# Kernel tuning notes

Measured on AMD Instinct MI355X. Metric: run time of the kernel, lower is better.

## Reference

```python
import jax, jax.numpy as jnp
import numpy as np

N0, N1, N2 = 120000, 24000, 6000  # nodes per sampled layer
H1, C1 = 8, 64   # layer1: heads, nhid (concat -> 512)
H2, C2 = 8, 256  # layer2: out heads, code_embed_dim (mean over heads)
D = 256
NEG_SLOPE = 0.2


def gat_conv(x_src, x_dst, src, dst, W, att_src, att_dst, bias, n_tgt, concat):
    H, C = att_src.shape
    h_src = (x_src @ W).reshape(-1, H, C)   # [N_src, H, C]
    h_dst = (x_dst @ W).reshape(-1, H, C)   # [N_tgt, H, C]
    a_src = jnp.einsum('nhc,hc->nh', h_src, att_src)  # [N_src, H]
    a_dst = jnp.einsum('nhc,hc->nh', h_dst, att_dst)  # [N_tgt, H]
    e = a_src[src] + a_dst[dst]                       # [E, H]
    e = jnp.where(e > 0, e, NEG_SLOPE * e)            # LeakyReLU
    # segment softmax over edges grouped by target node
    m = jax.ops.segment_max(e, dst, num_segments=n_tgt)  # [N_tgt, H]
    ex = jnp.exp(e - m[dst])
    denom = jax.ops.segment_sum(ex, dst, num_segments=n_tgt)
    alpha = ex / denom[dst]                           # [E, H]
    msg = alpha[:, :, None] * h_src[src]              # [E, H, C]
    out = jax.ops.segment_sum(msg, dst, num_segments=n_tgt)  # [N_tgt, H, C]
    if concat:
        return out.reshape(n_tgt, H * C) + bias
    return out.mean(axis=1) + bias


def setup_inputs() -> dict:
    key = jax.random.key(0)
    ks = jax.random.split(key, 12)
    E1, E2 = 384000, 96000
    g1 = 1.0 / np.sqrt(D)
    g2 = 1.0 / np.sqrt(H1 * C1)
    return {
        'x': jax.random.normal(ks[0], (N0, D), jnp.float32),
        'src1': jax.random.randint(ks[1], (E1,), 0, N0),
        'dst1': jax.random.randint(ks[2], (E1,), 0, N1),
        'src2': jax.random.randint(ks[3], (E2,), 0, N1),
        'dst2': jax.random.randint(ks[4], (E2,), 0, N2),
        'W1': jax.random.normal(ks[5], (D, H1 * C1), jnp.float32) * g1,
        'att_src1': jax.random.normal(ks[6], (H1, C1), jnp.float32) * 0.1,
        'att_dst1': jax.random.normal(ks[7], (H1, C1), jnp.float32) * 0.1,
        'b1': jnp.zeros((H1 * C1,), jnp.float32),
        'W2': jax.random.normal(ks[8], (H1 * C1, H2 * C2), jnp.float32) * g2,
        'att_src2': jax.random.normal(ks[9], (H2, C2), jnp.float32) * 0.1,
        'att_dst2': jax.random.normal(ks[10], (H2, C2), jnp.float32) * 0.1,
        'b2': jnp.zeros((C2,), jnp.float32),
    }


def reference(x, src1, dst1, src2, dst2, W1, att_src1, att_dst1, b1,
              W2, att_src2, att_dst2, b2):
    # layer 1: bipartite conv (x, x[:N1]), concat heads, then ELU
    x1 = gat_conv(x, x[:N1], src1, dst1, W1, att_src1, att_dst1, b1, N1, True)
    x1 = jax.nn.elu(x1)
    # layer 2: (x1, x1[:N2]), mean over heads
    x2 = gat_conv(x1, x1[:N2], src2, dst2, W2, att_src2, att_dst2, b2, N2, False)
    return x2
```

## Files before the change

### kernel.cpp

```cpp
#include <hip/hip_runtime.h>
#include <hip/hip_bf16.h>
#include <cstdint>

typedef __attribute__((ext_vector_type(8))) short short8;
typedef __attribute__((ext_vector_type(4))) float floatx4;
typedef __hip_bfloat16 bf16;
typedef unsigned short u16;

static constexpr int cN0 = 120000, cN1 = 24000, cN2 = 6000;
static constexpr int cD = 256, cHC1 = 512;
static constexpr int CH1 = 4800;

__device__ __forceinline__ float dot4(float4 a, float4 b) {
  return a.x * b.x + a.y * b.y + a.z * b.z + a.w * b.w;
}

__global__ __launch_bounds__(256)
void gat_w1t(const float* __restrict__ W1, u16* __restrict__ dst) {
  int t = blockIdx.x * 256 + threadIdx.x;
  if (t >= 512 * 256) return;
  int n = t >> 8, k = t & 255;
  bf16 v = bf16(W1[(size_t)k * 512 + n]);
  dst[t] = *(u16*)&v;
}

__global__ __launch_bounds__(256)
void gat_make_w2te(const float* __restrict__ W2, u16* __restrict__ out) {
  __shared__ u16 tile[32][33];
  int kt = blockIdx.x * 32, ct = blockIdx.y * 32, h = blockIdx.z;
  int tx = threadIdx.x & 31, ty4 = (threadIdx.x >> 5) * 4;
#pragma unroll
  for (int i = 0; i < 4; i++) {
    int k = kt + ty4 + i, c = ct + tx;
    bf16 v = bf16(W2[(size_t)k * 2048 + h * 256 + c]);
    tile[ty4 + i][tx] = *(u16*)&v;
  }
  __syncthreads();
#pragma unroll
  for (int i = 0; i < 4; i++) {
    int c = ct + ty4 + i, k = kt + tx;
    out[(size_t)c * 4096 + h * 512 + k] = tile[tx][ty4 + i];
  }
}

__global__ __launch_bounds__(256)
void gat_make_watt(const float* __restrict__ W, const float* __restrict__ atts,
                   const float* __restrict__ attd, float* __restrict__ ws,
                   float* __restrict__ wd, int K, int Ch, int ldw) {
  int lane = threadIdx.x & 63;
  int task = blockIdx.x * 4 + (threadIdx.x >> 6);
  if (task >= 8 * K) return;
  int h = task / K, k = task - h * K;
  const float* Wr = W + (size_t)k * ldw + h * Ch;
  const float* as = atts + h * Ch;
  const float* ad = attd + h * Ch;
  float ss = 0.f, dd = 0.f;
  for (int c = lane; c < Ch; c += 64) {
    float wv = Wr[c];
    ss += wv * as[c];
    dd += wv * ad[c];
  }
#pragma unroll
  for (int o = 32; o; o >>= 1) { ss += __shfl_down(ss, o); dd += __shfl_down(dd, o); }
  if (lane == 0) { ws[task] = ss; wd[task] = dd; }
}

#define RSTAGE(HALF, MASK)                                              \
  {                                                                     \
    _Pragma("unroll") for (int j = 0; j < HALF; j++) {                  \
      float send = (lane & MASK) ? v[j] : v[j + HALF];                  \
      float rcv = __shfl_xor(send, MASK);                               \
      v[j] = ((lane & MASK) ? v[j + HALF] : v[j]) + rcv;                \
    }                                                                   \
  }

__global__ __launch_bounds__(256)
void gat_scores_reg(const float* __restrict__ x, const float* __restrict__ wsrc,
                    const float* __restrict__ wdst, float* __restrict__ a_s,
                    float* __restrict__ a_d, int M, int MD) {
  int lane = threadIdx.x & 63;
  int wv = (blockIdx.x * 256 + threadIdx.x) >> 6;
  int nw = (gridDim.x * 256) >> 6;
  float4 w[16];
#pragma unroll
  for (int j = 0; j < 8; j++) {
    w[j]     = *(const float4*)&wsrc[j * 256 + lane * 4];
    w[j + 8] = *(const float4*)&wdst[j * 256 + lane * 4];
  }
  for (int row = wv; row < M; row += nw) {
    float4 xv = *(const float4*)&x[(size_t)row * 256 + lane * 4];
    float v[16];
#pragma unroll
    for (int j = 0; j < 16; j++) v[j] = dot4(xv, w[j]);
    RSTAGE(8, 1) RSTAGE(4, 2) RSTAGE(2, 4) RSTAGE(1, 8)
    v[0] += __shfl_xor(v[0], 16);
    v[0] += __shfl_xor(v[0], 32);
    if (lane < 16) {
      int o = ((lane & 1) << 3) | ((lane & 2) << 1) | ((lane & 4) >> 1) | ((lane & 8) >> 3);
      if (o < 8) a_s[row * 8 + o] = v[0];
      else if (row < MD) a_d[row * 8 + (o - 8)] = v[0];
    }
  }
}

__global__ __launch_bounds__(256)
void gat_scores_w512(const float* __restrict__ x, const float* __restrict__ wsrc,
                     const float* __restrict__ wdst, float* __restrict__ a_s,
                     float* __restrict__ a_d, int M, int MD) {
  __shared__ float wl[16 * 512];
  int tid = threadIdx.x;
#pragma unroll
  for (int base = 0; base < 8192; base += 1024) {
    int idx = base + tid * 4;
    int j = idx >> 9, c = idx & 511;
    *(float4*)&wl[idx] = (j < 8) ? *(const float4*)&wsrc[j * 512 + c]
                                 : *(const float4*)&wdst[(j - 8) * 512 + c];
  }
  __syncthreads();
  int lane = tid & 63;
  int wv = (blockIdx.x * 256 + tid) >> 6;
  int nw = (gridDim.x * 256) >> 6;
  for (int row = wv; row < M; row += nw) {
    float4 xa = *(const float4*)&x[(size_t)row * 512 + lane * 4];
    float4 xb = *(const float4*)&x[(size_t)row * 512 + 256 + lane * 4];
    float v[16];
#pragma unroll
    for (int j = 0; j < 16; j++) {
      float4 wa = *(const float4*)&wl[j * 512 + lane * 4];
      float4 wb = *(const float4*)&wl[j * 512 + 256 + lane * 4];
      v[j] = dot4(xa, wa) + dot4(xb, wb);
    }
    RSTAGE(8, 1) RSTAGE(4, 2) RSTAGE(2, 4) RSTAGE(1, 8)
    v[0] += __shfl_xor(v[0], 16);
    v[0] += __shfl_xor(v[0], 32);
    if (lane < 16) {
      int o = ((lane & 1) << 3) | ((lane & 2) << 1) | ((lane & 4) >> 1) | ((lane & 8) >> 3);
      if (o < 8) a_s[row * 8 + o] = v[0];
      else if (row < MD) a_d[row * 8 + (o - 8)] = v[0];
    }
  }
}

__global__ __launch_bounds__(256)
void gat_hist(const int* __restrict__ dstv, int* __restrict__ cnt, int E) {
  int t = blockIdx.x * 256 + threadIdx.x;
  if (t < E) atomicAdd(&cnt[dstv[t]], 1);
}

__global__ __launch_bounds__(1024)
void gat_scan_excl(const int* __restrict__ cnt, int* __restrict__ off, int n) {
  __shared__ int wsum[16];
  __shared__ int carry_s;
  int t = threadIdx.x, lane = t & 63, wid = t >> 6;
  if (t == 0) carry_s = 0;
  __syncthreads();
  for (int base = 0; base < n; base += 1024) {
    int idx = base + t;
    int v = (idx < n) ? cnt[idx] : 0;
    int x = v;
#pragma unroll
    for (int d = 1; d < 64; d <<= 1) { int y = __shfl_up(x, d); if (lane >= d) x += y; }
    if (lane == 63) wsum[wid] = x;
    __syncthreads();
    if (t < 16) {
      int s = wsum[t];
#pragma unroll
      for (int d = 1; d < 16; d <<= 1) { int y = __shfl_up(s, d); if (t >= d) s += y; }
      wsum[t] = s;
    }
    __syncthreads();
    int prefix = carry_s + (wid ? wsum[wid - 1] : 0) + x - v;
    if (idx < n) off[idx] = prefix;
    int tot = wsum[15];
    __syncthreads();
    if (t == 0) carry_s += tot;
    __syncthreads();
  }
  if (threadIdx.x == 0) off[n] = carry_s;
}

__global__ __launch_bounds__(256)
void gat_scatter_edge(const int* __restrict__ src, const int* __restrict__ dstv,
                      const float* __restrict__ a_s, const float* __restrict__ a_d,
                      const int* __restrict__ off, int* __restrict__ cur,
                      int* __restrict__ srcs, float* __restrict__ exs, int E) {
  int t = blockIdx.x * 256 + threadIdx.x;
  if (t >= E) return;
  int s = src[t], d = dstv[t];
  int slot = off[d] + atomicAdd(&cur[d], 1);
  srcs[slot] = s;
  const float* as = a_s + (size_t)s * 8;
  const float* ad = a_d + (size_t)d * 8;
  float4 s0 = *(const float4*)as, s1 = *(const float4*)(as + 4);
  float4 d0 = *(const float4*)ad, d1 = *(const float4*)(ad + 4);
  float ev[8] = { s0.x + d0.x, s0.y + d0.y, s0.z + d0.z, s0.w + d0.w,
                  s1.x + d1.x, s1.y + d1.y, s1.z + d1.z, s1.w + d1.w };
  float exv[8];
#pragma unroll
  for (int h = 0; h < 8; h++) {
    float e = ev[h];
    e = e > 0.f ? e : 0.2f * e;
    exv[h] = expf(e);
  }
  float4* op = (float4*)(exs + (size_t)slot * 8);
  op[0] = make_float4(exv[0], exv[1], exv[2], exv[3]);
  op[1] = make_float4(exv[4], exv[5], exv[6], exv[7]);
}

__global__ __launch_bounds__(256)
void gat_denom(const float* __restrict__ exs, const int* __restrict__ off,
               float* __restrict__ den, int N) {
  int lane = threadIdx.x & 63;
  int d = blockIdx.x * 4 + (threadIdx.x >> 6);
  if (d >= N) return;
  int beg = off[d], end = off[d + 1];
  float s = 0.f;
  for (size_t idx = (size_t)beg * 8 + lane; idx < (size_t)end * 8; idx += 64)
    s += exs[idx];
#pragma unroll
  for (int o = 32; o >= 8; o >>= 1) s += __shfl_down(s, o);
  if (lane < 8) den[(size_t)d * 8 + lane] = s;
}

__global__ __launch_bounds__(256)
void gat_gather_in1(const float* __restrict__ x, const float* __restrict__ exs,
                    const float* __restrict__ den, const int* __restrict__ off,
                    const int* __restrict__ srcs, u16* __restrict__ agg, int d0) {
  int d = d0 + blockIdx.x, t = threadIdx.x;
  int beg = off[d], end = off[d + 1];
  float inv[8];
#pragma unroll
  for (int j = 0; j < 8; j++) inv[j] = 1.f / den[(size_t)d * 8 + j];
  float acc[8] = {};
  int s_n = 0;
  if (beg < end) s_n = srcs[beg];
  for (int i = beg; i < end; i++) {
    int s = s_n;
    if (i + 1 < end) s_n = srcs[i + 1];
    float4 e0 = *(const float4*)&exs[(size_t)i * 8];
    float4 e1 = *(const float4*)&exs[(size_t)i * 8 + 4];
    float xv = x[(size_t)s * cD + t];
    acc[0] += e0.x * inv[0] * xv; acc[1] += e0.y * inv[1] * xv;
    acc[2] += e0.z * inv[2] * xv; acc[3] += e0.w * inv[3] * xv;
    acc[4] += e1.x * inv[4] * xv; acc[5] += e1.y * inv[5] * xv;
    acc[6] += e1.z * inv[6] * xv; acc[7] += e1.w * inv[7] * xv;
  }
  u16* ap = agg + (size_t)blockIdx.x * 2048 + t;
#pragma unroll
  for (int j = 0; j < 8; j++) {
    bf16 v = bf16(acc[j]);
    ap[(size_t)j * 256] = *(u16*)&v;
  }
}

__global__ __launch_bounds__(256)
void gat_gather_in2(const float* __restrict__ x1, const float* __restrict__ exs,
                    const float* __restrict__ den, const int* __restrict__ off,
                    const int* __restrict__ srcs, u16* __restrict__ agg, int d0) {
  int d = d0 + blockIdx.x, t = threadIdx.x;
  int beg = off[d], end = off[d + 1];
  float inv[8];
#pragma unroll
  for (int j = 0; j < 8; j++) inv[j] = 1.f / den[(size_t)d * 8 + j];
  float acc0[8] = {}, acc1[8] = {};
  int s_n = 0;
  if (beg < end) s_n = srcs[beg];
  for (int i = beg; i < end; i++) {
    int s = s_n;
    if (i + 1 < end) s_n = srcs[i + 1];
    float4 e0 = *(const float4*)&exs[(size_t)i * 8];
    float4 e1 = *(const float4*)&exs[(size_t)i * 8 + 4];
    float al[8] = { e0.x * inv[0], e0.y * inv[1], e0.z * inv[2], e0.w * inv[3],
                    e1.x * inv[4], e1.y * inv[5], e1.z * inv[6], e1.w * inv[7] };
    float xv0 = x1[(size_t)s * cHC1 + t];
    float xv1 = x1[(size_t)s * cHC1 + t + 256];
#pragma unroll
    for (int j = 0; j < 8; j++) { acc0[j] += al[j] * xv0; acc1[j] += al[j] * xv1; }
  }
  u16* ap = agg + (size_t)blockIdx.x * 4096;
#pragma unroll
  for (int j = 0; j < 8; j++) {
    bf16 v0 = bf16(acc0[j]), v1 = bf16(acc1[j]);
    ap[(size_t)j * 512 + t]       = *(u16*)&v0;
    ap[(size_t)j * 512 + t + 256] = *(u16*)&v1;
  }
}

template<int BN, int EPI>
__global__ __launch_bounds__(256)
void gat_gemm(const u16* __restrict__ A, long lda, const u16* __restrict__ Bt, long ldb,
              float* __restrict__ C, long ldc, int M, int K,
              const float* __restrict__ bias, int zA, int zB, long zC, int zBias) {
  __shared__ __align__(16) u16 Al[64 * 64];
  __shared__ __align__(16) u16 Bl[BN * 64];
  const int tid = threadIdx.x;
  const int bm = blockIdx.x << 6;
  const int n0 = blockIdx.y * BN;
  const int z = blockIdx.z;
  const u16* Ab = A + (size_t)z * zA;
  const u16* Bb = Bt + (size_t)z * zB + (size_t)n0 * ldb;
  const int wid = tid >> 6, lane = tid & 63;
  const int wm = (wid & 1) << 5, wn = (wid >> 1) * (BN / 2);
  const int q = lane >> 4, r = lane & 15;
  constexpr int NJ = BN / 32;
  floatx4 acc[2][NJ] = {};
  const int arow = tid >> 3;
  const int chunk = tid & 7;
  const int acol = chunk << 3;
  for (int k0 = 0; k0 < K; k0 += 64) {
    __syncthreads();
#pragma unroll
    for (int rr = 0; rr < 2; rr++) {
      int row = arow + rr * 32;
      int gr = bm + row; if (gr >= M) gr = M - 1;
      *(uint4*)&Al[row * 64 + ((chunk ^ (row & 7)) << 3)] =
          *(const uint4*)&Ab[(size_t)gr * lda + k0 + acol];
    }
#pragma unroll
    for (int rr = 0; rr < BN / 32; rr++) {
      int row = arow + rr * 32;
      *(uint4*)&Bl[row * 64 + ((chunk ^ (row & 7)) << 3)] =
          *(const uint4*)&Bb[(size_t)row * ldb + k0 + acol];
    }
    __syncthreads();
#pragma unroll
    for (int kk = 0; kk < 64; kk += 32) {
      const int cs = (((kk >> 3) + q) ^ (r & 7)) << 3;
      short8 af[2], bfr[NJ];
#pragma unroll
      for (int i = 0; i < 2; i++)  af[i]  = *(const short8*)&Al[(wm + i * 16 + r) * 64 + cs];
#pragma unroll
      for (int j = 0; j < NJ; j++) bfr[j] = *(const short8*)&Bl[(wn + j * 16 + r) * 64 + cs];
#pragma unroll
      for (int i = 0; i < 2; i++)
#pragma unroll
        for (int j = 0; j < NJ; j++)
          acc[i][j] = __builtin_amdgcn_mfma_f32_16x16x32_bf16(af[i], bfr[j], acc[i][j], 0, 0, 0);
    }
  }
#pragma unroll
  for (int i = 0; i < 2; i++)
#pragma unroll
    for (int j = 0; j < NJ; j++) {
      int gn = n0 + wn + j * 16 + r;
      float bv = (EPI == 1) ? bias[zBias * z + gn] : 0.f;
#pragma unroll
      for (int t2 = 0; t2 < 4; t2++) {
        int gm = bm + wm + i * 16 + q * 4 + t2;
        if (gm < M) {
          float v = acc[i][j][t2];
          if (EPI == 1) { v += bv; v = v > 0.f ? v : expm1f(v); }
          C[(size_t)z * zC + (size_t)gm * ldc + gn] = v;
        }
      }
    }
}

__global__ __launch_bounds__(256)
void gat_reduce4(const float* __restrict__ p, const float* __restrict__ bias,
                 float* __restrict__ out, int MN) {
  int t = blockIdx.x * 256 + threadIdx.x;
  if (t >= MN) return;
  size_t mn = (size_t)MN;
  float v = p[t] + p[t + mn] + p[t + 2 * mn] + p[t + 3 * mn];
  out[t] = v * 0.125f + bias[t & 255];
}

extern "C" void kernel_launch(void* const* d_in, const int* in_sizes, int n_in,
                              void* d_out, int out_size, void* d_ws, size_t ws_size,
                              hipStream_t stream) {
  const float* x    = (const float*)d_in[0];
  const int* src1   = (const int*)d_in[1];
  const int* dst1   = (const int*)d_in[2];
  const int* src2   = (const int*)d_in[3];
  const int* dst2   = (const int*)d_in[4];
  const float* W1   = (const float*)d_in[5];
  const float* atts1 = (const float*)d_in[6];
  const float* attd1 = (const float*)d_in[7];
  const float* b1   = (const float*)d_in[8];
  const float* W2   = (const float*)d_in[9];
  const float* atts2 = (const float*)d_in[10];
  const float* attd2 = (const float*)d_in[11];
  const float* b2   = (const float*)d_in[12];
  const int E1 = in_sizes[1], E2 = in_sizes[3];

  uint8_t* p = (uint8_t*)d_ws;
  auto alloc = [&](size_t b) { uint8_t* r = p; p += (b + 255) & ~(size_t)255; return r; };
  auto al = [](size_t b) { return (b + 255) & ~(size_t)255; };
  float* x1   = (float*)alloc((size_t)cN1 * cHC1 * 4);
  u16*   W1t  = (u16*)alloc((size_t)512 * 256 * 2);
  u16*   W2te = (u16*)alloc((size_t)256 * 4096 * 2);
  float* wts1 = (float*)alloc(8 * 256 * 4);
  float* wtd1 = (float*)alloc(8 * 256 * 4);
  float* wts2 = (float*)alloc(8 * 512 * 4);
  float* wtd2 = (float*)alloc(8 * 512 * 4);
  uint8_t* scratch = p;
  u16*   aggA  = (u16*)alloc((size_t)CH1 * 2048 * 2);
  float* a_s1  = (float*)alloc((size_t)cN0 * 32);
  float* a_d1  = (float*)alloc((size_t)cN1 * 32);
  float* exs1  = (float*)alloc((size_t)E1 * 32);
  int*   srcs1 = (int*)alloc((size_t)E1 * 4);
  int*   off1  = (int*)alloc((size_t)(cN1 + 1) * 4);
  float* den1  = (float*)alloc((size_t)cN1 * 32);
  uint8_t* zA = p;
  int*   cnt1 = (int*)alloc((size_t)cN1 * 4);
  int*   cur1 = (int*)alloc((size_t)cN1 * 4);
  size_t zAbytes = (size_t)(p - zA);

  size_t fixedB = al((size_t)cN1 * 32) + al((size_t)cN2 * 32) + al((size_t)E2 * 32) +
                  al((size_t)E2 * 4) + al((size_t)(cN2 + 1) * 4) + al((size_t)cN2 * 32) +
                  2 * al((size_t)cN2 * 4);
  size_t usedPersist = (size_t)(scratch - (uint8_t*)d_ws);
  int M2 = 6000;
  if (usedPersist + al((size_t)6000 * 4096 * 2) + al(4ull * 6000 * 256 * 4) + fixedB > ws_size)
    M2 = 3000;
  int nch2 = 6000 / M2;
  p = scratch;
  u16*   aggB  = (u16*)alloc((size_t)M2 * 4096 * 2);
  float* pbuf  = (float*)alloc(4ull * M2 * 256 * 4);
  float* a_s2  = (float*)alloc((size_t)cN1 * 32);
  float* a_d2  = (float*)alloc((size_t)cN2 * 32);
  float* exs2  = (float*)alloc((size_t)E2 * 32);
  int*   srcs2 = (int*)alloc((size_t)E2 * 4);
  int*   off2  = (int*)alloc((size_t)(cN2 + 1) * 4);
  float* den2  = (float*)alloc((size_t)cN2 * 32);
  uint8_t* zB = p;
  int*   cnt2 = (int*)alloc((size_t)cN2 * 4);
  int*   cur2 = (int*)alloc((size_t)cN2 * 4);
  size_t zBbytes = (size_t)(p - zB);

  gat_w1t<<<(512 * 256 + 255) / 256, 256, 0, stream>>>(W1, W1t);
  gat_make_w2te<<<dim3(16, 8, 8), 256, 0, stream>>>(W2, W2te);
  gat_make_watt<<<2 * 256, 256, 0, stream>>>(W1, atts1, attd1, wts1, wtd1, 256, 64, 512);
  gat_make_watt<<<2 * 512, 256, 0, stream>>>(W2, atts2, attd2, wts2, wtd2, 512, 256, 2048);

  hipMemsetAsync(zA, 0, zAbytes, stream);
  gat_scores_reg<<<1024, 256, 0, stream>>>(x, wts1, wtd1, a_s1, a_d1, cN0, cN1);
  gat_hist<<<(E1 + 255) / 256, 256, 0, stream>>>(dst1, cnt1, E1);
  gat_scan_excl<<<1, 1024, 0, stream>>>(cnt1, off1, cN1);
  gat_scatter_edge<<<(E1 + 255) / 256, 256, 0, stream>>>(src1, dst1, a_s1, a_d1, off1, cur1, srcs1, exs1, E1);
  gat_denom<<<(cN1 + 3) / 4, 256, 0, stream>>>(exs1, off1, den1, cN1);
  for (int c = 0; c < cN1 / CH1; c++) {
    int d0 = c * CH1;
    gat_gather_in1<<<CH1, 256, 0, stream>>>(x, exs1, den1, off1, srcs1, aggA, d0);
    gat_gemm<64, 1><<<dim3(CH1 / 64, 1, 8), 256, 0, stream>>>(
        aggA, 2048, W1t, 256, x1 + (size_t)d0 * cHC1, cHC1,
        CH1, 256, b1, 256, 64 * 256, 64, 64);
  }

  hipMemsetAsync(zB, 0, zBbytes, stream);
  gat_scores_w512<<<512, 256, 0, stream>>>(x1, wts2, wtd2, a_s2, a_d2, cN1, cN2);
  gat_hist<<<(E2 + 255) / 256, 256, 0, stream>>>(dst2, cnt2, E2);
  gat_scan_excl<<<1, 1024, 0, stream>>>(cnt2, off2, cN2);
  gat_scatter_edge<<<(E2 + 255) / 256, 256, 0, stream>>>(src2, dst2, a_s2, a_d2, off2, cur2, srcs2, exs2, E2);
  gat_denom<<<(cN2 + 3) / 4, 256, 0, stream>>>(exs2, off2, den2, cN2);
  for (int c = 0; c < nch2; c++) {
    int d0 = c * M2;
    gat_gather_in2<<<M2, 256, 0, stream>>>(x1, exs2, den2, off2, srcs2, aggB, d0);
    gat_gemm<64, 0><<<dim3((M2 + 63) / 64, 4, 4), 256, 0, stream>>>(
        aggB, 4096, W2te, 4096, pbuf, 256,
        M2, 1024, nullptr, 1024, 1024, (long)M2 * 256, 0);
    gat_reduce4<<<(M2 * 256 + 255) / 256, 256, 0, stream>>>(
        pbuf, b2, (float*)d_out + (size_t)d0 * 256, M2 * 256);
  }
}
```

Measured before the change: 600.5 us.

## Parallelize scan, fuse softmax denominator into gather, unroll edges, enlarge chunks

Replaces the single-block serial prefix scan with a three-kernel multi-block scan. Drops the separate denominator kernel and accumulates the softmax denominator inside the gather loops, which now process two edges per iteration for more memory-level parallelism. Layer 1 runs as a single chunk when the workspace allows it, cutting launch count, and the layer-2 GEMM uses a 128-wide N tile. The cost is more registers in the gather kernels, plus a dependence on the workspace size check for the larger buffers.

```diff
diff --git a/kernel.cpp b/kernel.cpp
--- a/kernel.cpp
+++ b/kernel.cpp
@@ -148,35 +148,44 @@
 }
 
 __global__ __launch_bounds__(1024)
-void gat_scan_excl(const int* __restrict__ cnt, int* __restrict__ off, int n) {
+void gat_scan1(const int* __restrict__ cnt, int* __restrict__ off,
+               int* __restrict__ bsum, int n) {
   __shared__ int wsum[16];
-  __shared__ int carry_s;
   int t = threadIdx.x, lane = t & 63, wid = t >> 6;
-  if (t == 0) carry_s = 0;
+  int idx = blockIdx.x * 1024 + t;
+  int v = (idx < n) ? cnt[idx] : 0;
+  int x = v;
+#pragma unroll
+  for (int d = 1; d < 64; d <<= 1) { int y = __shfl_up(x, d); if (lane >= d) x += y; }
+  if (lane == 63) wsum[wid] = x;
   __syncthreads();
-  for (int base = 0; base < n; base += 1024) {
-    int idx = base + t;
-    int v = (idx < n) ? cnt[idx] : 0;
-    int x = v;
-#pragma unroll
-    for (int d = 1; d < 64; d <<= 1) { int y = __shfl_up(x, d); if (lane >= d) x += y; }
-    if (lane == 63) wsum[wid] = x;
-    __syncthreads();
-    if (t < 16) {
-      int s = wsum[t];
-#pragma unroll
-      for (int d = 1; d < 16; d <<= 1) { int y = __shfl_up(s, d); if (t >= d) s += y; }
-      wsum[t] = s;
-    }
-    __syncthreads();
-    int prefix = carry_s + (wid ? wsum[wid - 1] : 0) + x - v;
-    if (idx < n) off[idx] = prefix;
-    int tot = wsum[15];
-    __syncthreads();
-    if (t == 0) carry_s += tot;
-    __syncthreads();
-  }
-  if (threadIdx.x == 0) off[n] = carry_s;
+  if (t < 16) {
+    int s = wsum[t];
+#pragma unroll
+    for (int d = 1; d < 16; d <<= 1) { int y = __shfl_up(s, d); if (t >= d) s += y; }
+    wsum[t] = s;
+  }
+  __syncthreads();
+  int excl = (wid ? wsum[wid - 1] : 0) + x - v;
+  if (idx < n) off[idx] = excl;
+  if (t == 1023) bsum[blockIdx.x] = wsum[15];
+}
+
+__global__ __launch_bounds__(64)
+void gat_scan2(int* __restrict__ bsum, int nb, int* __restrict__ off, int n) {
+  int t = threadIdx.x;
+  int v = (t < nb) ? bsum[t] : 0;
+  int x = v;
+#pragma unroll
+  for (int d = 1; d < 64; d <<= 1) { int y = __shfl_up(x, d); if (t >= d) x += y; }
+  if (t < nb) bsum[t] = x - v;
+  if (t == 63) off[n] = x;
+}
+
+__global__ __launch_bounds__(256)
+void gat_scan3(int* __restrict__ off, const int* __restrict__ bsum, int n) {
+  int i = blockIdx.x * 256 + threadIdx.x;
+  if (i < n) off[i] += bsum[i >> 10];
 }
 
 __global__ __launch_bounds__(256)
@@ -208,79 +217,89 @@
 }
 
 __global__ __launch_bounds__(256)
-void gat_denom(const float* __restrict__ exs, const int* __restrict__ off,
-               float* __restrict__ den, int N) {
-  int lane = threadIdx.x & 63;
-  int d = blockIdx.x * 4 + (threadIdx.x >> 6);
-  if (d >= N) return;
-  int beg = off[d], end = off[d + 1];
-  float s = 0.f;
-  for (size_t idx = (size_t)beg * 8 + lane; idx < (size_t)end * 8; idx += 64)
-    s += exs[idx];
-#pragma unroll
-  for (int o = 32; o >= 8; o >>= 1) s += __shfl_down(s, o);
-  if (lane < 8) den[(size_t)d * 8 + lane] = s;
-}
-
-__global__ __launch_bounds__(256)
 void gat_gather_in1(const float* __restrict__ x, const float* __restrict__ exs,
-                    const float* __restrict__ den, const int* __restrict__ off,
-                    const int* __restrict__ srcs, u16* __restrict__ agg, int d0) {
+                    const int* __restrict__ off, const int* __restrict__ srcs,
+                    u16* __restrict__ agg, int d0) {
   int d = d0 + blockIdx.x, t = threadIdx.x;
   int beg = off[d], end = off[d + 1];
-  float inv[8];
-#pragma unroll
-  for (int j = 0; j < 8; j++) inv[j] = 1.f / den[(size_t)d * 8 + j];
-  float acc[8] = {};
-  int s_n = 0;
-  if (beg < end) s_n = srcs[beg];
-  for (int i = beg; i < end; i++) {
-    int s = s_n;
-    if (i + 1 < end) s_n = srcs[i + 1];
-    float4 e0 = *(const float4*)&exs[(size_t)i * 8];
-    float4 e1 = *(const float4*)&exs[(size_t)i * 8 + 4];
+  float acc[8] = {}, den[8] = {};
+  int i = beg;
+  if ((end - beg) & 1) {
+    int s = srcs[i];
+    float ea[8];
+    *(float4*)&ea[0] = *(const float4*)&exs[(size_t)i * 8];
+    *(float4*)&ea[4] = *(const float4*)&exs[(size_t)i * 8 + 4];
     float xv = x[(size_t)s * cD + t];
-    acc[0] += e0.x * inv[0] * xv; acc[1] += e0.y * inv[1] * xv;
-    acc[2] += e0.z * inv[2] * xv; acc[3] += e0.w * inv[3] * xv;
-    acc[4] += e1.x * inv[4] * xv; acc[5] += e1.y * inv[5] * xv;
-    acc[6] += e1.z * inv[6] * xv; acc[7] += e1.w * inv[7] * xv;
+#pragma unroll
+    for (int j = 0; j < 8; j++) { acc[j] += ea[j] * xv; den[j] += ea[j]; }
+    i++;
+  }
+  for (; i < end; i += 2) {
+    int s0 = srcs[i], s1 = srcs[i + 1];
+    float ea[8], eb[8];
+    *(float4*)&ea[0] = *(const float4*)&exs[(size_t)i * 8];
+    *(float4*)&ea[4] = *(const float4*)&exs[(size_t)i * 8 + 4];
+    *(float4*)&eb[0] = *(const float4*)&exs[(size_t)(i + 1) * 8];
+    *(float4*)&eb[4] = *(const float4*)&exs[(size_t)(i + 1) * 8 + 4];
+    float xv0 = x[(size_t)s0 * cD + t];
+    float xv1 = x[(size_t)s1 * cD + t];
+#pragma unroll
+    for (int j = 0; j < 8; j++) {
+      acc[j] += ea[j] * xv0 + eb[j] * xv1;
+      den[j] += ea[j] + eb[j];
+    }
   }
   u16* ap = agg + (size_t)blockIdx.x * 2048 + t;
 #pragma unroll
   for (int j = 0; j < 8; j++) {
-    bf16 v = bf16(acc[j]);
+    float inv = den[j] > 0.f ? 1.f / den[j] : 0.f;
+    bf16 v = bf16(acc[j] * inv);
     ap[(size_t)j * 256] = *(u16*)&v;
   }
 }
 
 __global__ __launch_bounds__(256)
 void gat_gather_in2(const float* __restrict__ x1, const float* __restrict__ exs,
-                    const float* __restrict__ den, const int* __restrict__ off,
-                    const int* __restrict__ srcs, u16* __restrict__ agg, int d0) {
+                    const int* __restrict__ off, const int* __restrict__ srcs,
+                    u16* __restrict__ agg, int d0) {
   int d = d0 + blockIdx.x, t = threadIdx.x;
   int beg = off[d], end = off[d + 1];
-  float inv[8];
-#pragma unroll
-  for (int j = 0; j < 8; j++) inv[j] = 1.f / den[(size_t)d * 8 + j];
-  float acc0[8] = {}, acc1[8] = {};
-  int s_n = 0;
-  if (beg < end) s_n = srcs[beg];
-  for (int i = beg; i < end; i++) {
-    int s = s_n;
-    if (i + 1 < end) s_n = srcs[i + 1];
-    float4 e0 = *(const float4*)&exs[(size_t)i * 8];
-    float4 e1 = *(const float4*)&exs[(size_t)i * 8 + 4];
-    float al[8] = { e0.x * inv[0], e0.y * inv[1], e0.z * inv[2], e0.w * inv[3],
-                    e1.x * inv[4], e1.y * inv[5], e1.z * inv[6], e1.w * inv[7] };
-    float xv0 = x1[(size_t)s * cHC1 + t];
-    float xv1 = x1[(size_t)s * cHC1 + t + 256];
-#pragma unroll
-    for (int j = 0; j < 8; j++) { acc0[j] += al[j] * xv0; acc1[j] += al[j] * xv1; }
+  float acc0[8] = {}, acc1[8] = {}, den[8] = {};
+  int i = beg;
+  if ((end - beg) & 1) {
+    int s = srcs[i];
+    float ea[8];
+    *(float4*)&ea[0] = *(const float4*)&exs[(size_t)i * 8];
+    *(float4*)&ea[4] = *(const float4*)&exs[(size_t)i * 8 + 4];
+    float xa = x1[(size_t)s * cHC1 + t];
+    float xb = x1[(size_t)s * cHC1 + t + 256];
+#pragma unroll
+    for (int j = 0; j < 8; j++) { acc0[j] += ea[j] * xa; acc1[j] += ea[j] * xb; den[j] += ea[j]; }
+    i++;
+  }
+  for (; i < end; i += 2) {
+    int s0 = srcs[i], s1 = srcs[i + 1];
+    float ea[8], eb[8];
+    *(float4*)&ea[0] = *(const float4*)&exs[(size_t)i * 8];
+    *(float4*)&ea[4] = *(const float4*)&exs[(size_t)i * 8 + 4];
+    *(float4*)&eb[0] = *(const float4*)&exs[(size_t)(i + 1) * 8];
+    *(float4*)&eb[4] = *(const float4*)&exs[(size_t)(i + 1) * 8 + 4];
+    float xa0 = x1[(size_t)s0 * cHC1 + t];
+    float xb0 = x1[(size_t)s0 * cHC1 + t + 256];
+    float xa1 = x1[(size_t)s1 * cHC1 + t];
+    float xb1 = x1[(size_t)s1 * cHC1 + t + 256];
+#pragma unroll
+    for (int j = 0; j < 8; j++) {
+      acc0[j] += ea[j] * xa0 + eb[j] * xa1;
+      acc1[j] += ea[j] * xb0 + eb[j] * xb1;
+      den[j] += ea[j] + eb[j];
+    }
   }
   u16* ap = agg + (size_t)blockIdx.x * 4096;
 #pragma unroll
   for (int j = 0; j < 8; j++) {
-    bf16 v0 = bf16(acc0[j]), v1 = bf16(acc1[j]);
+    float inv = den[j] > 0.f ? 1.f / den[j] : 0.f;
+    bf16 v0 = bf16(acc0[j] * inv), v1 = bf16(acc1[j] * inv);
     ap[(size_t)j * 512 + t]       = *(u16*)&v0;
     ap[(size_t)j * 512 + t + 256] = *(u16*)&v1;
   }
@@ -395,25 +414,33 @@
   float* wts2 = (float*)alloc(8 * 512 * 4);
   float* wtd2 = (float*)alloc(8 * 512 * 4);
   uint8_t* scratch = p;
-  u16*   aggA  = (u16*)alloc((size_t)CH1 * 2048 * 2);
+  size_t usedPersist = (size_t)(scratch - (uint8_t*)d_ws);
+
+  auto phaseA = [&](size_t m1) {
+    return al(m1 * 2048 * 2) + al((size_t)cN0 * 32) + al((size_t)cN1 * 32) +
+           al((size_t)E1 * 32) + al((size_t)E1 * 4) + al((size_t)(cN1 + 1) * 4) +
+           al(256) + 2 * al((size_t)cN1 * 4);
+  };
+  int M1 = (usedPersist + phaseA(cN1) <= ws_size) ? cN1 : CH1;
+  int nch1 = cN1 / M1;
+  u16*   aggA  = (u16*)alloc((size_t)M1 * 2048 * 2);
   float* a_s1  = (float*)alloc((size_t)cN0 * 32);
   float* a_d1  = (float*)alloc((size_t)cN1 * 32);
   float* exs1  = (float*)alloc((size_t)E1 * 32);
   int*   srcs1 = (int*)alloc((size_t)E1 * 4);
   int*   off1  = (int*)alloc((size_t)(cN1 + 1) * 4);
-  float* den1  = (float*)alloc((size_t)cN1 * 32);
+  int*   bsum1 = (int*)alloc(256);
   uint8_t* zA = p;
   int*   cnt1 = (int*)alloc((size_t)cN1 * 4);
   int*   cur1 = (int*)alloc((size_t)cN1 * 4);
   size_t zAbytes = (size_t)(p - zA);
 
-  size_t fixedB = al((size_t)cN1 * 32) + al((size_t)cN2 * 32) + al((size_t)E2 * 32) +
-                  al((size_t)E2 * 4) + al((size_t)(cN2 + 1) * 4) + al((size_t)cN2 * 32) +
-                  2 * al((size_t)cN2 * 4);
-  size_t usedPersist = (size_t)(scratch - (uint8_t*)d_ws);
-  int M2 = 6000;
-  if (usedPersist + al((size_t)6000 * 4096 * 2) + al(4ull * 6000 * 256 * 4) + fixedB > ws_size)
-    M2 = 3000;
+  auto phaseB = [&](size_t m2) {
+    return al(m2 * 4096 * 2) + al(4ull * m2 * 256 * 4) + al((size_t)cN1 * 32) +
+           al((size_t)cN2 * 32) + al((size_t)E2 * 32) + al((size_t)E2 * 4) +
+           al((size_t)(cN2 + 1) * 4) + al(256) + 2 * al((size_t)cN2 * 4);
+  };
+  int M2 = (usedPersist + phaseB(6000) <= ws_size) ? 6000 : 3000;
   int nch2 = 6000 / M2;
   p = scratch;
   u16*   aggB  = (u16*)alloc((size_t)M2 * 4096 * 2);
@@ -423,7 +450,7 @@
   float* exs2  = (float*)alloc((size_t)E2 * 32);
   int*   srcs2 = (int*)alloc((size_t)E2 * 4);
   int*   off2  = (int*)alloc((size_t)(cN2 + 1) * 4);
-  float* den2  = (float*)alloc((size_t)cN2 * 32);
+  int*   bsum2 = (int*)alloc(256);
   uint8_t* zB = p;
   int*   cnt2 = (int*)alloc((size_t)cN2 * 4);
   int*   cur2 = (int*)alloc((size_t)cN2 * 4);
@@ -437,27 +464,35 @@
   hipMemsetAsync(zA, 0, zAbytes, stream);
   gat_scores_reg<<<1024, 256, 0, stream>>>(x, wts1, wtd1, a_s1, a_d1, cN0, cN1);
   gat_hist<<<(E1 + 255) / 256, 256, 0, stream>>>(dst1, cnt1, E1);
-  gat_scan_excl<<<1, 1024, 0, stream>>>(cnt1, off1, cN1);
+  {
+    int nb = (cN1 + 1023) / 1024;
+    gat_scan1<<<nb, 1024, 0, stream>>>(cnt1, off1, bsum1, cN1);
+    gat_scan2<<<1, 64, 0, stream>>>(bsum1, nb, off1, cN1);
+    gat_scan3<<<(cN1 + 255) / 256, 256, 0, stream>>>(off1, bsum1, cN1);
+  }
   gat_scatter_edge<<<(E1 + 255) / 256, 256, 0, stream>>>(src1, dst1, a_s1, a_d1, off1, cur1, srcs1, exs1, E1);
-  gat_denom<<<(cN1 + 3) / 4, 256, 0, stream>>>(exs1, off1, den1, cN1);
-  for (int c = 0; c < cN1 / CH1; c++) {
-    int d0 = c * CH1;
-    gat_gather_in1<<<CH1, 256, 0, stream>>>(x, exs1, den1, off1, srcs1, aggA, d0);
-    gat_gemm<64, 1><<<dim3(CH1 / 64, 1, 8), 256, 0, stream>>>(
+  for (int c = 0; c < nch1; c++) {
+    int d0 = c * M1;
+    gat_gather_in1<<<M1, 256, 0, stream>>>(x, exs1, off1, srcs1, aggA, d0);
+    gat_gemm<64, 1><<<dim3(M1 / 64, 1, 8), 256, 0, stream>>>(
         aggA, 2048, W1t, 256, x1 + (size_t)d0 * cHC1, cHC1,
-        CH1, 256, b1, 256, 64 * 256, 64, 64);
+        M1, 256, b1, 256, 64 * 256, 64, 64);
   }
 
   hipMemsetAsync(zB, 0, zBbytes, stream);
   gat_scores_w512<<<512, 256, 0, stream>>>(x1, wts2, wtd2, a_s2, a_d2, cN1, cN2);
   gat_hist<<<(E2 + 255) / 256, 256, 0, stream>>>(dst2, cnt2, E2);
-  gat_scan_excl<<<1, 1024, 0, stream>>>(cnt2, off2, cN2);
+  {
+    int nb = (cN2 + 1023) / 1024;
+    gat_scan1<<<nb, 1024, 0, stream>>>(cnt2, off2, bsum2, cN2);
+    gat_scan2<<<1, 64, 0, stream>>>(bsum2, nb, off2, cN2);
+    gat_scan3<<<(cN2 + 255) / 256, 256, 0, stream>>>(off2, bsum2, cN2);
+  }
   gat_scatter_edge<<<(E2 + 255) / 256, 256, 0, stream>>>(src2, dst2, a_s2, a_d2, off2, cur2, srcs2, exs2, E2);
-  gat_denom<<<(cN2 + 3) / 4, 256, 0, stream>>>(exs2, off2, den2, cN2);
   for (int c = 0; c < nch2; c++) {
     int d0 = c * M2;
-    gat_gather_in2<<<M2, 256, 0, stream>>>(x1, exs2, den2, off2, srcs2, aggB, d0);
-    gat_gemm<64, 0><<<dim3((M2 + 63) / 64, 4, 4), 256, 0, stream>>>(
+    gat_gather_in2<<<M2, 256, 0, stream>>>(x1, exs2, off2, srcs2, aggB, d0);
+    gat_gemm<128, 0><<<dim3((M2 + 63) / 64, 2, 4), 256, 0, stream>>>(
         aggB, 4096, W2te, 4096, pbuf, 256,
         M2, 1024, nullptr, 1024, 1024, (long)M2 * 256, 0);
     gat_reduce4<<<(M2 * 256 + 255) / 256, 256, 0, stream>>>(
```

New measurement: 495.4 us. 1.21x faster.
